# Optimization experiments

Hardware: AMD Instinct MI355X
Metric: run time of the kernel (lower is better)

The kernel has to match this reference:

```python
import jax, jax.numpy as jnp
import numpy as np

B, C, CI, T, H, W = 4, 256, 128, 8, 28, 28
EPS = 1e-5


def setup_inputs() -> dict:
    key = jax.random.key(0)
    ks = jax.random.split(key, 12)
    s = 0.02
    return {
        "x": jax.random.normal(ks[0], (B, C, T, H, W), jnp.float32),
        "Wg": jax.random.normal(ks[1], (CI, C), jnp.float32) * s,
        "bg": jax.random.normal(ks[2], (CI,), jnp.float32) * s,
        "Wt": jax.random.normal(ks[3], (CI, C), jnp.float32) * s,
        "bt": jax.random.normal(ks[4], (CI,), jnp.float32) * s,
        "Wp": jax.random.normal(ks[5], (CI, C), jnp.float32) * s,
        "bp": jax.random.normal(ks[6], (CI,), jnp.float32) * s,
        "Ww": jax.random.normal(ks[7], (C, CI), jnp.float32) * s,
        "bw": jax.random.normal(ks[8], (C,), jnp.float32) * s,
        "gamma": jax.random.normal(ks[9], (C,), jnp.float32) * s + 1.0,
        "beta": jax.random.normal(ks[10], (C,), jnp.float32) * s,
        "rmean": jax.random.normal(ks[11], (C,), jnp.float32) * s,
        "rvar": jax.random.uniform(jax.random.fold_in(key, 99), (C,), jnp.float32, 0.5, 1.5),
    }


def reference(x, Wg, bg, Wt, bt, Wp, bp, Ww, bw, gamma, beta, rmean, rvar):
    b, c, t, h, w = x.shape
    n = t * h * w
    xf = x.reshape(b, c, n)                                   # [B,C,N]
    # 1x1x1 conv projections == per-position linear maps
    g = jnp.einsum('oc,bcn->bno', Wg, xf) + bg                # [B,N,Ci]
    th = jnp.einsum('oc,bcn->bno', Wt, xf) + bt               # [B,N,Ci]
    ph = jnp.einsum('oc,bcn->bon', Wp, xf) + bp[None, :, None]  # [B,Ci,N]
    f = jnp.einsum('bnc,bcm->bnm', th, ph)                    # [B,N,N] attention logits
    attn = jax.nn.softmax(f, axis=-1)
    y = jnp.einsum('bnm,bmo->bno', attn, g)                   # [B,N,Ci]
    wy = jnp.einsum('co,bno->bcn', Ww, y) + bw[None, :, None]  # [B,C,N]
    # BatchNorm3d (eval mode: running stats)
    inv = gamma / jnp.sqrt(rvar + EPS)
    wy = wy * inv[None, :, None] + (beta - rmean * inv)[None, :, None]
    z = wy + xf                                               # residual
    return z.reshape(b, c, t, h, w)
```

## Files before the change

kernel.cpp:

```cpp
#include <hip/hip_runtime.h>
#include <hip/hip_bf16.h>
#include <hip/hip_fp8.h>

#define BB 4
#define CC 256
#define CI 128
#define NN 6272
#define LOG2E 1.4426950408889634f

typedef __attribute__((ext_vector_type(8))) __bf16 bf16x8;
typedef __attribute__((ext_vector_type(4))) float f32x4;
typedef __attribute__((ext_vector_type(16))) float f32x16;

__device__ __forceinline__ unsigned cvtpk_fp8(float a, float b) {
  unsigned r;
  asm("v_cvt_pk_fp8_f32 %0, %1, %2" : "=v"(r) : "v"(a), "v"(b));
  return r;
}

__device__ __forceinline__ unsigned char to_fp8(float v) {
  __hip_fp8_e4m3 t(v);
  return *reinterpret_cast<unsigned char*>(&t);
}

__device__ __forceinline__ float fexp2(float s) {
  float t = (s + 127.0f) * 8388608.0f;
  return __int_as_float((int)t);
}

__global__ void nlb_prep(const float* __restrict__ Wg, const float* __restrict__ bg,
                         const float* __restrict__ Wt, const float* __restrict__ bt,
                         const float* __restrict__ Wp, const float* __restrict__ bp,
                         const float* __restrict__ Ww, const float* __restrict__ bw,
                         const float* __restrict__ gamma, const float* __restrict__ beta,
                         const float* __restrict__ rmean, const float* __restrict__ rvar,
                         __bf16* __restrict__ wall, float* __restrict__ ball,
                         __bf16* __restrict__ wwb, float* __restrict__ scale,
                         float* __restrict__ shift) {
  int idx = blockIdx.x * 256 + threadIdx.x;
  if (idx < 384 * 256) {
    int o = idx >> 8, c = idx & 255;
    float v, bv;
    if (o < 128)      { v = Wt[o * 256 + c] * LOG2E;  bv = bt[o] * LOG2E; }
    else if (o < 256) { v = Wp[(o - 128) * 256 + c]; bv = bp[o - 128]; }
    else              { v = Wg[(o - 256) * 256 + c]; bv = bg[o - 256]; }
    wall[idx] = (__bf16)v;
    if (c == 0) ball[o] = bv;
  } else if (idx < 384 * 256 + 256 * 128) {
    int i = idx - 384 * 256;
    wwb[i] = (__bf16)Ww[i];
  } else if (idx < 384 * 256 + 256 * 128 + 256) {
    int c = idx - (384 * 256 + 256 * 128);
    float inv = gamma[c] * rsqrtf(rvar[c] + 1e-5f);
    scale[c] = inv;
    shift[c] = (bw[c] - rmean[c]) * inv + beta[c];
  }
}

__launch_bounds__(256)
__global__ void nlb_proj(const float* __restrict__ x, const __bf16* __restrict__ wall,
                         const float* __restrict__ ball,
                         unsigned char* __restrict__ Q8, unsigned char* __restrict__ KF,
                         unsigned char* __restrict__ VF) {
  const int nb = blockIdx.x;
  const int b  = blockIdx.y;
  const int tid = threadIdx.x;
  const int lane = tid & 63, w = tid >> 6;
  const int n0 = nb * 64;
  const int r = lane & 15, g = lane >> 4;

  __shared__ __bf16 xl[64][40];

  const float* xb = x + (size_t)b * CC * NN;
  f32x4 acc[6][4] = {};

  const int snn = tid & 63;
  const int skg = tid >> 6;

  for (int k0 = 0; k0 < 256; k0 += 32) {
    bf16x8 tmp;
#pragma unroll
    for (int i = 0; i < 8; ++i)
      tmp[i] = (__bf16)xb[(size_t)(k0 + skg * 8 + i) * NN + n0 + snn];
    __syncthreads();
    *reinterpret_cast<bf16x8*>(&xl[snn][skg * 8]) = tmp;
    __syncthreads();

    bf16x8 bfrag[4];
#pragma unroll
    for (int j = 0; j < 4; ++j)
      bfrag[j] = *reinterpret_cast<const bf16x8*>(&xl[j * 16 + r][g * 8]);
#pragma unroll
    for (int mb = 0; mb < 6; ++mb) {
      bf16x8 afrag = *reinterpret_cast<const bf16x8*>(
          &wall[(size_t)(mb * 64 + w * 16 + r) * 256 + k0 + g * 8]);
#pragma unroll
      for (int j = 0; j < 4; ++j)
        acc[mb][j] = __builtin_amdgcn_mfma_f32_16x16x32_bf16(afrag, bfrag[j], acc[mb][j], 0, 0, 0);
    }
  }

  unsigned char* KFb = KF + (size_t)b * NN * CI;
  unsigned char* VFb = VF + (size_t)b * NN * CI;
#pragma unroll
  for (int mb = 0; mb < 6; ++mb) {
    const int m0 = mb * 64 + w * 16;
    if (m0 < 128) {
#pragma unroll
      for (int j = 0; j < 4; ++j) {
        int n = n0 + j * 16 + r;
        union { unsigned char bch[4]; unsigned u; } pk;
#pragma unroll
        for (int reg = 0; reg < 4; ++reg)
          pk.bch[reg] = to_fp8(acc[mb][j][reg] + ball[m0 + g * 4 + reg]);
        *reinterpret_cast<unsigned*>(&Q8[((size_t)b * NN + n) * CI + m0 + g * 4]) = pk.u;
      }
    } else if (m0 < 256) {
      const int kc = (m0 - 128) >> 4;
#pragma unroll
      for (int j = 0; j < 4; ++j) {
        int n = n0 + j * 16 + r;
        union { unsigned char bch[4]; unsigned u; } pk;
#pragma unroll
        for (int reg = 0; reg < 4; ++reg)
          pk.bch[reg] = to_fp8(acc[mb][j][reg] + ball[m0 + g * 4 + reg]);
        *reinterpret_cast<unsigned*>(
            &KFb[(size_t)(n >> 5) * 4096 + kc * 512 + (g >> 1) * 256 + (n & 31) * 8 + (g & 1) * 4]) = pk.u;
      }
    } else {
#pragma unroll
      for (int j = 0; j < 4; ++j) {
        int n = n0 + j * 16 + r;
        const int g32 = n >> 5, kl = n & 31;
        const int ch = kl >> 4, khi = (kl >> 3) & 1, kb = kl & 7;
#pragma unroll
        for (int reg = 0; reg < 4; ++reg) {
          int o = m0 + g * 4 + reg;
          int ci = o - 256, cb = ci >> 5, cc = ci & 31;
          float v = acc[mb][j][reg] + ball[o];
          VFb[(size_t)g32 * 4096 + (ch * 4 + cb) * 512 + khi * 256 + cc * 8 + kb] = to_fp8(v);
        }
      }
    }
  }
}

__launch_bounds__(256, 2)
__global__ void nlb_attn(const unsigned char* __restrict__ Q8,
                         const unsigned char* __restrict__ KF,
                         const unsigned char* __restrict__ VF,
                         __bf16* __restrict__ Yp, float* __restrict__ Lp) {
  const int bid = blockIdx.x;
  const int pair = bid & 7;
  const int b = pair >> 1, kh = pair & 1;
  const int q32 = bid >> 3;
  const int tid = threadIdx.x, lane = tid & 63, w = tid >> 6;
  const int c = lane & 31, hi = lane >> 5;
  const int q0 = q32 * 32;

  const int t0 = kh * 98 + ((w * 98) >> 2);
  const int t1 = kh * 98 + (((w + 1) * 98) >> 2);
  const int NT = t1 - t0;

  const unsigned char* Qb = Q8 + (size_t)b * NN * CI;
  const char* kfp = (const char*)(KF + (size_t)b * NN * CI) + (size_t)t0 * 4096;
  const char* vfp = (const char*)(VF + (size_t)b * NN * CI) + (size_t)t0 * 4096;

  __shared__ float scr[4096];
  __shared__ float mls[64];

  long qf[8];
#pragma unroll
  for (int kc = 0; kc < 8; ++kc)
    qf[kc] = *reinterpret_cast<const long*>(&Qb[(size_t)(q0 + c) * CI + kc * 16 + hi * 8]);

  long kf[8], vf[8];
#pragma unroll
  for (int kc = 0; kc < 8; ++kc)
    kf[kc] = *reinterpret_cast<const long*>(kfp + kc * 512 + lane * 8);
#pragma unroll
  for (int i = 0; i < 8; ++i)
    vf[i] = *reinterpret_cast<const long*>(vfp + i * 512 + lane * 8);

  f32x16 yacc[4] = {};
  float l_acc = 0.f;

  for (int t = 0; t < NT; ++t) {
    f32x16 sA, sB;
#pragma unroll
    for (int i = 0; i < 16; ++i) { sA[i] = -4.f; sB[i] = 0.f; }
    __builtin_amdgcn_s_setprio(1);
#pragma unroll
    for (int kc = 0; kc < 4; ++kc) {
      sA = __builtin_amdgcn_mfma_f32_32x32x16_fp8_fp8(kf[kc], qf[kc], sA, 0, 0, 0);
      sB = __builtin_amdgcn_mfma_f32_32x32x16_fp8_fp8(kf[kc + 4], qf[kc + 4], sB, 0, 0, 0);
    }
    __builtin_amdgcn_s_setprio(0);

    if (t < NT - 1) {
      kfp += 4096;
#pragma unroll
      for (int kc = 0; kc < 8; ++kc)
        kf[kc] = *reinterpret_cast<const long*>(kfp + kc * 512 + lane * 8);
    }

    float s[16];
    float ps = 0.f;
#pragma unroll
    for (int reg = 0; reg < 16; ++reg) {
      s[reg] = fexp2(sA[reg] + sB[reg]);
      ps += s[reg];
    }
    l_acc += ps;

    unsigned pw[4];
#pragma unroll
    for (int i = 0; i < 4; ++i) {
      unsigned lo  = cvtpk_fp8(s[4 * i + 0], s[4 * i + 1]);
      unsigned hi2 = cvtpk_fp8(s[4 * i + 2], s[4 * i + 3]);
      pw[i] = __builtin_amdgcn_perm(hi2, lo, 0x05040100);
    }

    __builtin_amdgcn_s_setprio(1);
#pragma unroll
    for (int ch = 0; ch < 2; ++ch) {
      unsigned A = pw[ch * 2 + 0], B = pw[ch * 2 + 1];
      unsigned sX = (unsigned)__shfl_xor((int)(hi ? A : B), 32);
      unsigned plo = hi ? sX : A;
      unsigned phi = hi ? B : sX;
      long pa = (long)(((unsigned long long)phi << 32) | plo);
#pragma unroll
      for (int cb = 0; cb < 4; ++cb)
        yacc[cb] = __builtin_amdgcn_mfma_f32_32x32x16_fp8_fp8(pa, vf[ch * 4 + cb], yacc[cb], 0, 0, 0);
    }
    __builtin_amdgcn_s_setprio(0);

    if (t < NT - 1) {
      vfp += 4096;
#pragma unroll
      for (int i = 0; i < 8; ++i)
        vf[i] = *reinterpret_cast<const long*>(vfp + i * 512 + lane * 8);
    }
  }

  float l_full = l_acc + __shfl_xor(l_acc, 32);

#pragma unroll 1
  for (int src = 1; src < 4; ++src) {
    __syncthreads();
    if (w == src) {
#pragma unroll
      for (int cb = 0; cb < 4; ++cb)
#pragma unroll
        for (int reg = 0; reg < 16; ++reg)
          scr[(cb * 16 + reg) * 64 + lane] = yacc[cb][reg];
      mls[lane] = l_full;
    }
    __syncthreads();
    if (w == 0) {
#pragma unroll
      for (int cb = 0; cb < 4; ++cb)
#pragma unroll
        for (int reg = 0; reg < 16; ++reg)
          yacc[cb][reg] += scr[(cb * 16 + reg) * 64 + lane];
      l_full += mls[lane];
    }
  }
  if (w == 0) {
    if (hi == 0)
      Lp[(size_t)(kh * 4 + b) * NN + q0 + c] = l_full;
    __bf16* Yb = Yp + (size_t)(kh * 4 + b) * NN * CI;
#pragma unroll
    for (int cb = 0; cb < 4; ++cb) {
#pragma unroll
      for (int reg = 0; reg < 16; ++reg) {
        int qloc = (reg & 3) + 8 * (reg >> 2) + 4 * hi;
        Yb[(size_t)(q0 + qloc) * CI + cb * 32 + c] = (__bf16)yacc[cb][reg];
      }
    }
  }
}

__launch_bounds__(256)
__global__ void nlb_out(const __bf16* __restrict__ Yp, const float* __restrict__ Lp,
                        const __bf16* __restrict__ wwb,
                        const float* __restrict__ scale, const float* __restrict__ shift,
                        const float* __restrict__ x, float* __restrict__ out) {
  const int nb = blockIdx.x;
  const int mb = blockIdx.y;
  const int b  = blockIdx.z;
  const int tid = threadIdx.x, lane = tid & 63, w = tid >> 6;
  const int r = lane & 15, g = lane >> 4;
  const int n0 = nb * 64, c0 = mb * 64 + w * 16;

  const __bf16* Y0 = Yp + (size_t)b * NN * CI;
  const __bf16* Y1 = Yp + (size_t)(4 + b) * NN * CI;
  f32x4 acc[4] = {};
#pragma unroll
  for (int k0 = 0; k0 < 128; k0 += 32) {
    bf16x8 af = *reinterpret_cast<const bf16x8*>(&wwb[(size_t)(c0 + r) * CI + k0 + g * 8]);
#pragma unroll
    for (int j = 0; j < 4; ++j) {
      size_t yoff = (size_t)(n0 + j * 16 + r) * CI + k0 + g * 8;
      bf16x8 bf0 = *reinterpret_cast<const bf16x8*>(&Y0[yoff]);
      acc[j] = __builtin_amdgcn_mfma_f32_16x16x32_bf16(af, bf0, acc[j], 0, 0, 0);
      bf16x8 bf1 = *reinterpret_cast<const bf16x8*>(&Y1[yoff]);
      acc[j] = __builtin_amdgcn_mfma_f32_16x16x32_bf16(af, bf1, acc[j], 0, 0, 0);
    }
  }
  const float* xb = x + (size_t)b * CC * NN;
  float* ob = out + (size_t)b * CC * NN;
#pragma unroll
  for (int j = 0; j < 4; ++j) {
    int n = n0 + j * 16 + r;
    float il = 1.f / (Lp[(size_t)b * NN + n] + Lp[(size_t)(4 + b) * NN + n]);
#pragma unroll
    for (int reg = 0; reg < 4; ++reg) {
      int cc = c0 + g * 4 + reg;
      size_t off = (size_t)cc * NN + n;
      ob[off] = acc[j][reg] * (il * scale[cc]) + shift[cc] + xb[off];
    }
  }
}

extern "C" void kernel_launch(void* const* d_in, const int* in_sizes, int n_in,
                              void* d_out, int out_size, void* d_ws, size_t ws_size,
                              hipStream_t stream) {
  (void)in_sizes; (void)n_in; (void)out_size; (void)ws_size;
  const float* x     = (const float*)d_in[0];
  const float* Wg    = (const float*)d_in[1];
  const float* bg    = (const float*)d_in[2];
  const float* Wt    = (const float*)d_in[3];
  const float* bt    = (const float*)d_in[4];
  const float* Wp    = (const float*)d_in[5];
  const float* bp    = (const float*)d_in[6];
  const float* Ww    = (const float*)d_in[7];
  const float* bw    = (const float*)d_in[8];
  const float* gamma = (const float*)d_in[9];
  const float* beta  = (const float*)d_in[10];
  const float* rmean = (const float*)d_in[11];
  const float* rvar  = (const float*)d_in[12];
  float* out = (float*)d_out;

  char* ws = (char*)d_ws;
  __bf16* wall = (__bf16*)(ws + 0);
  float*  ball = (float*)(ws + 196608);
  __bf16* wwb  = (__bf16*)(ws + 198144);
  float*  scl  = (float*)(ws + 263680);
  float*  shf  = (float*)(ws + 264704);
  unsigned char* Q8 = (unsigned char*)(ws + 265728);
  unsigned char* KF = (unsigned char*)(ws + 3476992);
  unsigned char* VF = (unsigned char*)(ws + 6688256);
  __bf16* Yp   = (__bf16*)(ws + 9899520);
  float*  Lp   = (float*)(ws + 22744576);

  nlb_prep<<<513, 256, 0, stream>>>(Wg, bg, Wt, bt, Wp, bp, Ww, bw, gamma, beta,
                                    rmean, rvar, wall, ball, wwb, scl, shf);
  nlb_proj<<<dim3(98, 4), 256, 0, stream>>>(x, wall, ball, Q8, KF, VF);
  nlb_attn<<<1568, 256, 0, stream>>>(Q8, KF, VF, Yp, Lp);
  nlb_out<<<dim3(98, 4, 4), 256, 0, stream>>>(Yp, Lp, wwb, scl, shf, x, out);
}
```

Baseline: 176.5 us.

## Software-pipeline QK scores one tile ahead and drop P shuffle via V layout

Computes the QK^T scores for the next key tile before doing the softmax/PV step of the current tile, so score MFMAs overlap with exp and PV work and with the K prefetch running two tiles ahead. The V fragment layout written in the projection kernel is permuted so the packed fp8 probabilities can feed the PV MFMA directly, removing the cross-half lane shuffle. The -4 bias that was folded into the accumulator init now sits in the exp2 bit trick constant (123 instead of 127), and the loop is unrolled by two. In exchange it holds an extra score accumulator in registers, which adds register pressure under the two-blocks-per-CU launch bound.

```diff
diff --git a/kernel.cpp b/kernel.cpp
--- a/kernel.cpp
+++ b/kernel.cpp
@@ -23,8 +23,8 @@
   return *reinterpret_cast<unsigned char*>(&t);
 }
 
-__device__ __forceinline__ float fexp2(float s) {
-  float t = (s + 127.0f) * 8388608.0f;
+__device__ __forceinline__ float fexp2m(float s) {
+  float t = (s + 123.0f) * 8388608.0f;
   return __int_as_float((int)t);
 }
 
@@ -132,7 +132,8 @@
       for (int j = 0; j < 4; ++j) {
         int n = n0 + j * 16 + r;
         const int g32 = n >> 5, kl = n & 31;
-        const int ch = kl >> 4, khi = (kl >> 3) & 1, kb = kl & 7;
+        const int ch = kl >> 4, m = kl & 15;
+        const int khi = (m >> 2) & 1, kb = (m & 3) + 4 * (m >> 3);
 #pragma unroll
         for (int reg = 0; reg < 4; ++reg) {
           int o = m0 + g * 4 + reg;
@@ -159,8 +160,7 @@
   const int q0 = q32 * 32;
 
   const int t0 = kh * 98 + ((w * 98) >> 2);
-  const int t1 = kh * 98 + (((w + 1) * 98) >> 2);
-  const int NT = t1 - t0;
+  const int NT = (kh * 98 + (((w + 1) * 98) >> 2)) - t0;
 
   const unsigned char* Qb = Q8 + (size_t)b * NN * CI;
   const char* kfp = (const char*)(KF + (size_t)b * NN * CI) + (size_t)t0 * 4096;
@@ -178,69 +178,77 @@
 #pragma unroll
   for (int kc = 0; kc < 8; ++kc)
     kf[kc] = *reinterpret_cast<const long*>(kfp + kc * 512 + lane * 8);
+
+  f32x16 sP = {};
+#pragma unroll
+  for (int kc = 0; kc < 8; ++kc)
+    sP = __builtin_amdgcn_mfma_f32_32x32x16_fp8_fp8(kf[kc], qf[kc], sP, 0, 0, 0);
+
 #pragma unroll
   for (int i = 0; i < 8; ++i)
     vf[i] = *reinterpret_cast<const long*>(vfp + i * 512 + lane * 8);
+  if (NT > 1) {
+    kfp += 4096;
+#pragma unroll
+    for (int kc = 0; kc < 8; ++kc)
+      kf[kc] = *reinterpret_cast<const long*>(kfp + kc * 512 + lane * 8);
+  }
 
   f32x16 yacc[4] = {};
   float l_acc = 0.f;
 
+#pragma unroll 2
   for (int t = 0; t < NT; ++t) {
-    f32x16 sA, sB;
-#pragma unroll
-    for (int i = 0; i < 16; ++i) { sA[i] = -4.f; sB[i] = 0.f; }
-    __builtin_amdgcn_s_setprio(1);
-#pragma unroll
-    for (int kc = 0; kc < 4; ++kc) {
-      sA = __builtin_amdgcn_mfma_f32_32x32x16_fp8_fp8(kf[kc], qf[kc], sA, 0, 0, 0);
-      sB = __builtin_amdgcn_mfma_f32_32x32x16_fp8_fp8(kf[kc + 4], qf[kc + 4], sB, 0, 0, 0);
-    }
-    __builtin_amdgcn_s_setprio(0);
-
-    if (t < NT - 1) {
+    f32x16 sN = {};
+    if (t + 1 < NT) {
+      __builtin_amdgcn_s_setprio(1);
+#pragma unroll
+      for (int kc = 0; kc < 8; ++kc)
+        sN = __builtin_amdgcn_mfma_f32_32x32x16_fp8_fp8(kf[kc], qf[kc], sN, 0, 0, 0);
+      __builtin_amdgcn_s_setprio(0);
+    }
+    if (t + 2 < NT) {
       kfp += 4096;
 #pragma unroll
       for (int kc = 0; kc < 8; ++kc)
         kf[kc] = *reinterpret_cast<const long*>(kfp + kc * 512 + lane * 8);
     }
 
-    float s[16];
+    float s16[16];
     float ps = 0.f;
 #pragma unroll
     for (int reg = 0; reg < 16; ++reg) {
-      s[reg] = fexp2(sA[reg] + sB[reg]);
-      ps += s[reg];
+      s16[reg] = fexp2m(sP[reg]);
+      ps += s16[reg];
     }
     l_acc += ps;
 
     unsigned pw[4];
 #pragma unroll
     for (int i = 0; i < 4; ++i) {
-      unsigned lo  = cvtpk_fp8(s[4 * i + 0], s[4 * i + 1]);
-      unsigned hi2 = cvtpk_fp8(s[4 * i + 2], s[4 * i + 3]);
+      unsigned lo  = cvtpk_fp8(s16[4 * i + 0], s16[4 * i + 1]);
+      unsigned hi2 = cvtpk_fp8(s16[4 * i + 2], s16[4 * i + 3]);
       pw[i] = __builtin_amdgcn_perm(hi2, lo, 0x05040100);
     }
 
     __builtin_amdgcn_s_setprio(1);
 #pragma unroll
     for (int ch = 0; ch < 2; ++ch) {
-      unsigned A = pw[ch * 2 + 0], B = pw[ch * 2 + 1];
-      unsigned sX = (unsigned)__shfl_xor((int)(hi ? A : B), 32);
-      unsigned plo = hi ? sX : A;
-      unsigned phi = hi ? B : sX;
-      long pa = (long)(((unsigned long long)phi << 32) | plo);
+      long pa = (long)(((unsigned long long)pw[ch * 2 + 1] << 32) | pw[ch * 2]);
 #pragma unroll
       for (int cb = 0; cb < 4; ++cb)
         yacc[cb] = __builtin_amdgcn_mfma_f32_32x32x16_fp8_fp8(pa, vf[ch * 4 + cb], yacc[cb], 0, 0, 0);
     }
     __builtin_amdgcn_s_setprio(0);
 
-    if (t < NT - 1) {
+    if (t + 1 < NT) {
       vfp += 4096;
 #pragma unroll
       for (int i = 0; i < 8; ++i)
         vf[i] = *reinterpret_cast<const long*>(vfp + i * 512 + lane * 8);
     }
+
+    sP = sN;
   }
 
   float l_full = l_acc + __shfl_xor(l_acc, 32);
```

Result: no change. 174.8 us (-0.9%).
